# Optimization experiments

Measured on AMD Instinct MI355X. Metric: run time of the kernel, lower is better.

Reference implementation:

```python
import jax, jax.numpy as jnp
import numpy as np
from jax import lax

H = 128; NOISE = 128; L = 16; A = 10; HYB = 3; F_NODE = 17; E_FEAT = 4
TEMP = 1.0
MAX_VALENCES = jnp.array([4., 3., 2., 1., 4., 2., 6., 1., 4., 4.], dtype=jnp.float32)


def setup_inputs():
    key = jax.random.key(0)
    ks = jax.random.split(key, 16)
    B, N = 4096, 32
    def w(k, *s):
        return jax.random.normal(k, s, dtype=jnp.float32) * 0.05
    return {
        'noise': jax.random.normal(ks[0], (B, NOISE), dtype=jnp.float32),
        'w1': w(ks[1], NOISE, H), 'b1': jnp.zeros((H,), jnp.float32),
        'gat_w': w(ks[2], L, H, H), 'gat_b': jnp.zeros((L, H), jnp.float32),
        'att_src': w(ks[3], L, H), 'att_dst': w(ks[4], L, H),
        'w_atom': w(ks[5], H, A), 'b_atom': jnp.zeros((A,), jnp.float32),
        'w_hyb': w(ks[6], H, HYB), 'b_hyb': jnp.zeros((HYB,), jnp.float32),
        'w_deg': w(ks[7], H, 1), 'b_deg': jnp.zeros((1,), jnp.float32),
        'w_chg': w(ks[8], H, 1), 'b_chg': jnp.zeros((1,), jnp.float32),
        'w_arom': w(ks[9], H, 1), 'b_arom': jnp.zeros((1,), jnp.float32),
        'w_eex': w(ks[10], 2 * F_NODE, 1), 'b_eex': jnp.zeros((1,), jnp.float32),
        'w_ety': w(ks[11], 2 * F_NODE, E_FEAT), 'b_ety': jnp.zeros((E_FEAT,), jnp.float32),
        'batch_size': B, 'num_nodes': N,
    }


def _gumbel(k, shape):
    u = jax.random.uniform(k, shape, minval=1e-6, maxval=1.0 - 1e-6)
    return -jnp.log(-jnp.log(u))


def reference(noise, w1, b1, gat_w, gat_b, att_src, att_dst, w_atom, b_atom,
              w_hyb, b_hyb, w_deg, b_deg, w_chg, b_chg, w_arom, b_arom,
              w_eex, b_eex, w_ety, b_ety, batch_size, num_nodes):
    B, N = batch_size, num_nodes
    h0 = jax.nn.relu(noise @ w1 + b1)                      # [B,H]
    x = jnp.broadcast_to(h0[:, None, :], (B, N, h0.shape[-1]))
    idx = jnp.arange(N)
    # chain adjacency (both directions) + self loops (PyG GATConv default)
    adj = (jnp.abs(idx[:, None] - idx[None, :]) == 1) | (idx[:, None] == idx[None, :])
    neg = jnp.float32(-1e9)

    def layer(xc, p):
        W, b, a_s, a_d = p
        h = xc @ W + b                                     # [B,N,H]
        e_src = h @ a_s                                    # [B,N]
        e_dst = h @ a_d
        s = jax.nn.leaky_relu(e_dst[:, :, None] + e_src[:, None, :], 0.2)  # [B,N,N]
        s = jnp.where(adj, s, neg)
        alpha = jax.nn.softmax(s, axis=-1)
        out = jnp.einsum('bij,bjh->bih', alpha, h)
        return jax.nn.relu(out + xc), None                 # residual GAT layer

    x, _ = lax.scan(layer, x, (gat_w, gat_b, att_src, att_dst))

    sk = jax.random.split(jax.random.key(42), 4)
    # atom type head + categorical sampling (Gumbel-max on logits/T)
    atom_logits = x @ w_atom + b_atom                      # [B,N,A]
    atom_lp = jax.nn.log_softmax(atom_logits, axis=-1)
    atom_idx = jnp.argmax(atom_logits / TEMP + _gumbel(sk[0], atom_logits.shape), axis=-1)
    atom_lp_mol = jnp.take_along_axis(atom_lp, atom_idx[..., None], axis=-1)[..., 0].mean(axis=1)
    # hybridization head
    hyb_logits = x @ w_hyb + b_hyb                         # [B,N,3]
    hyb_lp = jax.nn.log_softmax(hyb_logits, axis=-1)
    hyb_idx = jnp.argmax(hyb_logits / TEMP + _gumbel(sk[1], hyb_logits.shape), axis=-1)
    hyb_lp_mol = jnp.take_along_axis(hyb_lp, hyb_idx[..., None], axis=-1)[..., 0].mean(axis=1)
    # remaining node heads
    deg = jax.nn.sigmoid(x @ w_deg + b_deg)
    chg = jnp.tanh(lax.stop_gradient(x @ w_chg + b_chg))   # .clone().detach() in torch
    arom_p = jax.nn.sigmoid(x @ w_arom + b_arom)
    arom = (jax.random.uniform(sk[2], arom_p.shape) < arom_p).astype(jnp.float32)
    val = (MAX_VALENCES[atom_idx] / 5.0)[..., None]
    node_features = jnp.concatenate([
        jax.nn.one_hot(atom_idx, A, dtype=jnp.float32), deg, chg,
        jax.nn.one_hot(hyb_idx, HYB, dtype=jnp.float32), arom, val], axis=-1)  # [B,N,17]
    # edge heads on chain edges (both directions)
    u = jnp.arange(N - 1); v = u + 1
    eu = jnp.concatenate([u, v]); ev = jnp.concatenate([v, u])
    ef = jnp.concatenate([node_features[:, eu], node_features[:, ev]], axis=-1)  # [B,2(N-1),34]
    exist_p = jax.nn.sigmoid(ef @ w_eex + b_eex)[..., 0]
    edge_mask = exist_p > 0.5
    type_logits = ef @ w_ety + b_ety
    type_idx = jnp.argmax(type_logits / TEMP + _gumbel(sk[3], type_logits.shape), axis=-1)
    edge_attr = jax.nn.one_hot(type_idx, E_FEAT, dtype=jnp.float32)
    return node_features, atom_lp_mol, hyb_lp_mol, edge_attr, edge_mask
```

## Files before the change

### kernel.cpp

```cpp
#include <hip/hip_runtime.h>
#include <stdint.h>
#include <math.h>


typedef double d4 __attribute__((ext_vector_type(4)));

struct U2 { uint32_t a, b; };

__device__ __forceinline__ U2 threefry(uint32_t k0, uint32_t k1, uint32_t x0, uint32_t x1) {
  const uint32_t ks2 = k0 ^ k1 ^ 0x1BD11BDAu;
#define TFR(r) { x0 += x1; x1 = (x1 << (r)) | (x1 >> (32 - (r))); x1 ^= x0; }
  x0 += k0;  x1 += k1;
  TFR(13) TFR(15) TFR(26) TFR(6)
  x0 += k1;  x1 += ks2 + 1u;
  TFR(17) TFR(29) TFR(16) TFR(24)
  x0 += ks2; x1 += k0 + 2u;
  TFR(13) TFR(15) TFR(26) TFR(6)
  x0 += k0;  x1 += k1 + 3u;
  TFR(17) TFR(29) TFR(16) TFR(24)
  x0 += k1;  x1 += ks2 + 4u;
  TFR(13) TFR(15) TFR(26) TFR(6)
  x0 += ks2; x1 += k0 + 5u;
#undef TFR
  U2 r; r.a = x0; r.b = x1; return r;
}

__device__ __forceinline__ uint32_t pbits(uint32_t k0, uint32_t k1, uint32_t ctr) {
  U2 r = threefry(k0, k1, 0u, ctr);
  return r.a ^ r.b;
}

__device__ __forceinline__ float bits_to_unit(uint32_t bits) {
  return __uint_as_float((bits >> 9) | 0x3f800000u) - 1.0f;
}

__device__ __forceinline__ float jgumbel(uint32_t k0, uint32_t k1, uint32_t ctr) {
  const float minv = 1e-6f;
  const float maxv = (float)(1.0 - 1e-6);
  const float span = maxv - minv;
  float f = bits_to_unit(pbits(k0, k1, ctr));
  float u = fmaxf(minv, __fadd_rn(__fmul_rn(f, span), minv));
  return -logf(-logf(u));
}

extern "C" __global__ void __launch_bounds__(256)
gen_kernel(const float* __restrict__ noise,
           const float* __restrict__ w1,
           const float* __restrict__ b1,
           const float* __restrict__ gat_w,
           const float* __restrict__ gat_b,
           const float* __restrict__ w_atom,
           const float* __restrict__ b_atom,
           const float* __restrict__ w_hyb,
           const float* __restrict__ b_hyb,
           const float* __restrict__ w_deg,
           const float* __restrict__ b_deg,
           const float* __restrict__ w_chg,
           const float* __restrict__ b_chg,
           const float* __restrict__ w_arom,
           const float* __restrict__ b_arom,
           const float* __restrict__ w_eex,
           const float* __restrict__ b_eex,
           const float* __restrict__ w_ety,
           const float* __restrict__ b_ety,
           float* __restrict__ out)
{
  __shared__ __align__(16) double sX[128][18];
  __shared__ double sScr[16][16];
  __shared__ float  sNF[16][32][17];
  __shared__ double sLP[16][64];

  const int t       = threadIdx.x;
  const int wv      = t >> 6;
  const int ln      = t & 63;
  const int g       = ln >> 4;
  const int i       = ln & 15;
  const int molBase = blockIdx.x * 16;
  const int colb    = wv << 5;

  int rowOf[4], colOf[4];
  {
    d4 z4 = {0.0, 0.0, 0.0, 0.0};
    const double selK0 = (g == 0) ? 1.0 : 0.0;
    const double idxv  = (double)i;
    d4 prow = __builtin_amdgcn_mfma_f64_16x16x4f64(idxv,  selK0, z4, 0, 0, 0);
    d4 pcol = __builtin_amdgcn_mfma_f64_16x16x4f64(selK0, idxv,  z4, 0, 0, 0);
    #pragma unroll
    for (int j = 0; j < 4; ++j) {
      rowOf[j] = (int)prow[j];
      colOf[j] = (int)pcol[j];
    }
  }

  #pragma unroll
  for (int it = 0; it < 8; ++it) {
    const int idx = t + (it << 8);
    const int c = idx & 127, m = idx >> 7;
    sX[c][m] = (double)noise[(((size_t)(molBase + m)) << 7) + c];
  }
  __syncthreads();

  #pragma unroll 1
  for (int l = 0; l < 17; ++l) {
    const float* __restrict__ W  = (l == 0) ? w1 : (gat_w + (((size_t)(l - 1)) << 14));
    const float* __restrict__ bp = (l == 0) ? b1 : (gat_b + ((l - 1) << 7));

    d4 acc0 = {0.0, 0.0, 0.0, 0.0};
    d4 acc1 = {0.0, 0.0, 0.0, 0.0};

    #pragma unroll
    for (int ks = 0; ks < 32; ++ks) {
      const int kk = (ks << 2) + g;
      const double a   = sX[kk][i];
      const double wb0 = (double)W[(kk << 7) + colb + i];
      const double wb1 = (double)W[(kk << 7) + colb + 16 + i];
      acc0 = __builtin_amdgcn_mfma_f64_16x16x4f64(a, wb0, acc0, 0, 0, 0);
      acc1 = __builtin_amdgcn_mfma_f64_16x16x4f64(a, wb1, acc1, 0, 0, 0);
    }

    double nv0[4], nv1[4];
    #pragma unroll
    for (int j = 0; j < 4; ++j) {
      const int cc0 = colb + colOf[j];
      const int cc1 = cc0 + 16;
      double t0 = acc0[j] + (double)bp[cc0];
      double t1 = acc1[j] + (double)bp[cc1];
      if (l > 0) {
        t0 += sX[cc0][rowOf[j]];
        t1 += sX[cc1][rowOf[j]];
      }
      nv0[j] = fmax(t0, 0.0);
      nv1[j] = fmax(t1, 0.0);
    }
    __syncthreads();
    #pragma unroll
    for (int j = 0; j < 4; ++j) {
      sX[colb + colOf[j]][rowOf[j]]      = nv0[j];
      sX[colb + 16 + colOf[j]][rowOf[j]] = nv1[j];
    }
    __syncthreads();
  }

  {
    const int mh = t >> 4;
    const int h  = t & 15;
    const float* wp; int stride; double bias;
    if (h < 10)       { wp = w_atom + h;        stride = 10; bias = (double)b_atom[h]; }
    else if (h < 13)  { wp = w_hyb + (h - 10);  stride = 3;  bias = (double)b_hyb[h - 10]; }
    else if (h == 13) { wp = w_deg;             stride = 1;  bias = (double)b_deg[0]; }
    else if (h == 14) { wp = w_chg;             stride = 1;  bias = (double)b_chg[0]; }
    else              { wp = w_arom;            stride = 1;  bias = (double)b_arom[0]; }
    double acc = 0.0;
    for (int c = 0; c < 128; ++c)
      acc = fma(sX[c][mh], (double)wp[c * stride], acc);
    sScr[mh][h] = acc + bias;
  }
  __syncthreads();

  const U2 k0p = threefry(0u, 42u, 0u, 0u);
  const U2 k1p = threefry(0u, 42u, 0u, 1u);
  const U2 k2p = threefry(0u, 42u, 0u, 2u);
  const U2 k3p = threefry(0u, 42u, 0u, 3u);

  for (int r = 0; r < 2; ++r) {
    const int mloc = (r << 3) + (t >> 5);
    const int n    = t & 31;
    const int mol  = molBase + mloc;
    const double* scr = sScr[mloc];

    double m = scr[0];
    #pragma unroll
    for (int a = 1; a < 10; ++a) m = fmax(m, scr[a]);
    double lsum = 0.0;
    #pragma unroll
    for (int a = 0; a < 10; ++a) lsum += exp(scr[a] - m);
    const double lse = log(lsum);
    const uint32_t abase = ((uint32_t)mol * 32u + (uint32_t)n) * 10u;
    int asel = 0; double abest = 0.0;
    #pragma unroll
    for (int a = 0; a < 10; ++a) {
      const double gg = (double)jgumbel(k0p.a, k0p.b, abase + (uint32_t)a);
      const double sc = scr[a] + gg;
      if (a == 0 || sc > abest) { abest = sc; asel = a; }
    }
    sLP[mloc][n] = (scr[asel] - m) - lse;

    double m2 = fmax(fmax(scr[10], scr[11]), scr[12]);
    double ls2 = exp(scr[10] - m2) + exp(scr[11] - m2) + exp(scr[12] - m2);
    const double lse2 = log(ls2);
    const uint32_t hbase = ((uint32_t)mol * 32u + (uint32_t)n) * 3u;
    int hsel = 0; double hbest = 0.0;
    #pragma unroll
    for (int j = 0; j < 3; ++j) {
      const double gg = (double)jgumbel(k1p.a, k1p.b, hbase + (uint32_t)j);
      const double sc = scr[10 + j] + gg;
      if (j == 0 || sc > hbest) { hbest = sc; hsel = j; }
    }
    sLP[mloc][32 + n] = (scr[10 + hsel] - m2) - lse2;

    const double deg = 1.0 / (1.0 + exp(-scr[13]));
    const double chg = tanh(scr[14]);
    const double pr  = 1.0 / (1.0 + exp(-scr[15]));
    const uint32_t ridx = (uint32_t)mol * 32u + (uint32_t)n;
    const double uu = (double)bits_to_unit(pbits(k2p.a, k2p.b, ridx));
    const double arom = (uu < pr) ? 1.0 : 0.0;
    const double valt[10] = {4.0/5.0, 3.0/5.0, 2.0/5.0, 1.0/5.0, 4.0/5.0,
                             2.0/5.0, 6.0/5.0, 1.0/5.0, 4.0/5.0, 4.0/5.0};
    double nf[17];
    #pragma unroll
    for (int q = 0; q < 10; ++q) nf[q] = (q == asel) ? 1.0 : 0.0;
    nf[10] = deg; nf[11] = chg;
    #pragma unroll
    for (int j = 0; j < 3; ++j) nf[12 + j] = (j == hsel) ? 1.0 : 0.0;
    nf[15] = arom; nf[16] = valt[asel];

    const size_t o = ((size_t)mol * 32 + n) * 17;
    #pragma unroll
    for (int q = 0; q < 17; ++q) {
      sNF[mloc][n][q] = (float)nf[q];
      out[o + q] = (float)nf[q];
    }
  }
  __syncthreads();

  #pragma unroll 1
  for (int r = 0; r < 4; ++r) {
    const int mloc = (r << 2) + wv;
    const int mol  = molBase + mloc;
    if (ln == 62) {
      double sa = 0.0;
      for (int n = 0; n < 32; ++n) sa += sLP[mloc][n];
      out[2228224 + (size_t)mol] = (float)(sa / 32.0);
    } else if (ln == 63) {
      double sh = 0.0;
      for (int n = 0; n < 32; ++n) sh += sLP[mloc][32 + n];
      out[2232320 + (size_t)mol] = (float)(sh / 32.0);
    } else {
      const int e = ln;
      const int nu_ = (e < 31) ? e : (e - 30);
      const int nv_ = (e < 31) ? (e + 1) : (e - 31);
      double lex = 0.0;
      double lt[4] = {0.0, 0.0, 0.0, 0.0};
      for (int q = 0; q < 17; ++q) {
        const double f = (double)sNF[mloc][nu_][q];
        lex = fma(f, (double)w_eex[q], lex);
        #pragma unroll
        for (int c = 0; c < 4; ++c) lt[c] = fma(f, (double)w_ety[q * 4 + c], lt[c]);
      }
      for (int q = 0; q < 17; ++q) {
        const double f = (double)sNF[mloc][nv_][q];
        lex = fma(f, (double)w_eex[17 + q], lex);
        #pragma unroll
        for (int c = 0; c < 4; ++c) lt[c] = fma(f, (double)w_ety[(17 + q) * 4 + c], lt[c]);
      }
      lex += (double)b_eex[0];
      #pragma unroll
      for (int c = 0; c < 4; ++c) lt[c] += (double)b_ety[c];

      const double pex = 1.0 / (1.0 + exp(-lex));
      out[3252224 + (size_t)mol * 62 + e] = (pex > 0.5) ? 1.f : 0.f;

      const uint32_t tbase = ((uint32_t)mol * 62u + (uint32_t)e) * 4u;
      int tsel = 0; double tbest = 0.0;
      #pragma unroll
      for (int c = 0; c < 4; ++c) {
        const double gg = (double)jgumbel(k3p.a, k3p.b, tbase + (uint32_t)c);
        const double sc = lt[c] + gg;
        if (c == 0 || sc > tbest) { tbest = sc; tsel = c; }
      }
      const size_t o = 2236416 + ((size_t)mol * 62 + e) * 4;
      #pragma unroll
      for (int c = 0; c < 4; ++c) out[o + c] = (c == tsel) ? 1.f : 0.f;
    }
  }
}

extern "C" void kernel_launch(void* const* d_in, const int* in_sizes, int n_in,
                              void* d_out, int out_size, void* d_ws, size_t ws_size,
                              hipStream_t stream) {
  (void)in_sizes; (void)n_in; (void)out_size; (void)d_ws; (void)ws_size;
  hipLaunchKernelGGL(gen_kernel, dim3(256), dim3(256), 0, stream,
                     (const float*)d_in[0],  (const float*)d_in[1],
                     (const float*)d_in[2],  (const float*)d_in[3],
                     (const float*)d_in[4],
                     (const float*)d_in[7],  (const float*)d_in[8],
                     (const float*)d_in[9],  (const float*)d_in[10],
                     (const float*)d_in[11], (const float*)d_in[12],
                     (const float*)d_in[13], (const float*)d_in[14],
                     (const float*)d_in[15], (const float*)d_in[16],
                     (const float*)d_in[17], (const float*)d_in[18],
                     (const float*)d_in[19], (const float*)d_in[20],
                     (float*)d_out);
}
```

Measured before the change: 186.3 us.

## Double the block to 512 threads and ping-pong the activation buffer

Each block now runs 8 wavefronts instead of 4. Each wave computes one 16-column MFMA tile per layer instead of two, which doubles the waves available to hide latency per block. The activation matrix is double-buffered in shared memory, so each layer needs one barrier instead of two and results are written directly without staging in registers. In exchange the block uses more LDS and threads, and the per-node and per-edge tail phases are reassigned across the larger thread count.

```diff
diff --git a/kernel.cpp b/kernel.cpp
--- a/kernel.cpp
+++ b/kernel.cpp
@@ -43,7 +43,7 @@
   return -logf(-logf(u));
 }
 
-extern "C" __global__ void __launch_bounds__(256)
+extern "C" __global__ void __launch_bounds__(512)
 gen_kernel(const float* __restrict__ noise,
            const float* __restrict__ w1,
            const float* __restrict__ b1,
@@ -65,7 +65,7 @@
            const float* __restrict__ b_ety,
            float* __restrict__ out)
 {
-  __shared__ __align__(16) double sX[128][18];
+  __shared__ __align__(16) double sX[2][128][18];
   __shared__ double sScr[16][16];
   __shared__ float  sNF[16][32][17];
   __shared__ double sLP[16][64];
@@ -76,7 +76,7 @@
   const int g       = ln >> 4;
   const int i       = ln & 15;
   const int molBase = blockIdx.x * 16;
-  const int colb    = wv << 5;
+  const int colb    = wv << 4;
 
   int rowOf[4], colOf[4];
   {
@@ -93,55 +93,42 @@
   }
 
   #pragma unroll
-  for (int it = 0; it < 8; ++it) {
-    const int idx = t + (it << 8);
+  for (int it = 0; it < 4; ++it) {
+    const int idx = t + (it << 9);
     const int c = idx & 127, m = idx >> 7;
-    sX[c][m] = (double)noise[(((size_t)(molBase + m)) << 7) + c];
+    sX[0][c][m] = (double)noise[(((size_t)(molBase + m)) << 7) + c];
   }
   __syncthreads();
 
+  int p = 0;
   #pragma unroll 1
   for (int l = 0; l < 17; ++l) {
     const float* __restrict__ W  = (l == 0) ? w1 : (gat_w + (((size_t)(l - 1)) << 14));
     const float* __restrict__ bp = (l == 0) ? b1 : (gat_b + ((l - 1) << 7));
-
-    d4 acc0 = {0.0, 0.0, 0.0, 0.0};
-    d4 acc1 = {0.0, 0.0, 0.0, 0.0};
+    const int q = p ^ 1;
+
+    d4 acc = {0.0, 0.0, 0.0, 0.0};
 
     #pragma unroll
     for (int ks = 0; ks < 32; ++ks) {
       const int kk = (ks << 2) + g;
-      const double a   = sX[kk][i];
-      const double wb0 = (double)W[(kk << 7) + colb + i];
-      const double wb1 = (double)W[(kk << 7) + colb + 16 + i];
-      acc0 = __builtin_amdgcn_mfma_f64_16x16x4f64(a, wb0, acc0, 0, 0, 0);
-      acc1 = __builtin_amdgcn_mfma_f64_16x16x4f64(a, wb1, acc1, 0, 0, 0);
-    }
-
-    double nv0[4], nv1[4];
+      const double a  = sX[p][kk][i];
+      const double wb = (double)W[(kk << 7) + colb + i];
+      acc = __builtin_amdgcn_mfma_f64_16x16x4f64(a, wb, acc, 0, 0, 0);
+    }
+
     #pragma unroll
     for (int j = 0; j < 4; ++j) {
-      const int cc0 = colb + colOf[j];
-      const int cc1 = cc0 + 16;
-      double t0 = acc0[j] + (double)bp[cc0];
-      double t1 = acc1[j] + (double)bp[cc1];
-      if (l > 0) {
-        t0 += sX[cc0][rowOf[j]];
-        t1 += sX[cc1][rowOf[j]];
-      }
-      nv0[j] = fmax(t0, 0.0);
-      nv1[j] = fmax(t1, 0.0);
+      const int cc = colb + colOf[j];
+      double tv = acc[j] + (double)bp[cc];
+      if (l > 0) tv += sX[p][cc][rowOf[j]];
+      sX[q][cc][rowOf[j]] = fmax(tv, 0.0);
     }
     __syncthreads();
-    #pragma unroll
-    for (int j = 0; j < 4; ++j) {
-      sX[colb + colOf[j]][rowOf[j]]      = nv0[j];
-      sX[colb + 16 + colOf[j]][rowOf[j]] = nv1[j];
-    }
-    __syncthreads();
-  }
-
-  {
+    p = q;
+  }
+
+  if (t < 256) {
     const int mh = t >> 4;
     const int h  = t & 15;
     const float* wp; int stride; double bias;
@@ -152,7 +139,7 @@
     else              { wp = w_arom;            stride = 1;  bias = (double)b_arom[0]; }
     double acc = 0.0;
     for (int c = 0; c < 128; ++c)
-      acc = fma(sX[c][mh], (double)wp[c * stride], acc);
+      acc = fma(sX[p][c][mh], (double)wp[c * stride], acc);
     sScr[mh][h] = acc + bias;
   }
   __syncthreads();
@@ -162,8 +149,8 @@
   const U2 k2p = threefry(0u, 42u, 0u, 2u);
   const U2 k3p = threefry(0u, 42u, 0u, 3u);
 
-  for (int r = 0; r < 2; ++r) {
-    const int mloc = (r << 3) + (t >> 5);
+  {
+    const int mloc = t >> 5;
     const int n    = t & 31;
     const int mol  = molBase + mloc;
     const double* scr = sScr[mloc];
@@ -208,7 +195,7 @@
                              2.0/5.0, 6.0/5.0, 1.0/5.0, 4.0/5.0, 4.0/5.0};
     double nf[17];
     #pragma unroll
-    for (int q = 0; q < 10; ++q) nf[q] = (q == asel) ? 1.0 : 0.0;
+    for (int q2 = 0; q2 < 10; ++q2) nf[q2] = (q2 == asel) ? 1.0 : 0.0;
     nf[10] = deg; nf[11] = chg;
     #pragma unroll
     for (int j = 0; j < 3; ++j) nf[12 + j] = (j == hsel) ? 1.0 : 0.0;
@@ -216,16 +203,16 @@
 
     const size_t o = ((size_t)mol * 32 + n) * 17;
     #pragma unroll
-    for (int q = 0; q < 17; ++q) {
-      sNF[mloc][n][q] = (float)nf[q];
-      out[o + q] = (float)nf[q];
+    for (int q2 = 0; q2 < 17; ++q2) {
+      sNF[mloc][n][q2] = (float)nf[q2];
+      out[o + q2] = (float)nf[q2];
     }
   }
   __syncthreads();
 
   #pragma unroll 1
-  for (int r = 0; r < 4; ++r) {
-    const int mloc = (r << 2) + wv;
+  for (int r = 0; r < 2; ++r) {
+    const int mloc = (r << 3) + wv;
     const int mol  = molBase + mloc;
     if (ln == 62) {
       double sa = 0.0;
@@ -241,17 +228,17 @@
       const int nv_ = (e < 31) ? (e + 1) : (e - 31);
       double lex = 0.0;
       double lt[4] = {0.0, 0.0, 0.0, 0.0};
-      for (int q = 0; q < 17; ++q) {
-        const double f = (double)sNF[mloc][nu_][q];
-        lex = fma(f, (double)w_eex[q], lex);
+      for (int q2 = 0; q2 < 17; ++q2) {
+        const double f = (double)sNF[mloc][nu_][q2];
+        lex = fma(f, (double)w_eex[q2], lex);
         #pragma unroll
-        for (int c = 0; c < 4; ++c) lt[c] = fma(f, (double)w_ety[q * 4 + c], lt[c]);
+        for (int c = 0; c < 4; ++c) lt[c] = fma(f, (double)w_ety[q2 * 4 + c], lt[c]);
       }
-      for (int q = 0; q < 17; ++q) {
-        const double f = (double)sNF[mloc][nv_][q];
-        lex = fma(f, (double)w_eex[17 + q], lex);
+      for (int q2 = 0; q2 < 17; ++q2) {
+        const double f = (double)sNF[mloc][nv_][q2];
+        lex = fma(f, (double)w_eex[17 + q2], lex);
         #pragma unroll
-        for (int c = 0; c < 4; ++c) lt[c] = fma(f, (double)w_ety[(17 + q) * 4 + c], lt[c]);
+        for (int c = 0; c < 4; ++c) lt[c] = fma(f, (double)w_ety[(17 + q2) * 4 + c], lt[c]);
       }
       lex += (double)b_eex[0];
       #pragma unroll
@@ -279,7 +266,7 @@
                               void* d_out, int out_size, void* d_ws, size_t ws_size,
                               hipStream_t stream) {
   (void)in_sizes; (void)n_in; (void)out_size; (void)d_ws; (void)ws_size;
-  hipLaunchKernelGGL(gen_kernel, dim3(256), dim3(256), 0, stream,
+  hipLaunchKernelGGL(gen_kernel, dim3(256), dim3(512), 0, stream,
                      (const float*)d_in[0],  (const float*)d_in[1],
                      (const float*)d_in[2],  (const float*)d_in[3],
                      (const float*)d_in[4],
```

After: 178.7 us. 4.1% less time.
